# Optimization experiments

Hardware: AMD Instinct MI355X
Metric: run time of the kernel (lower is better)

Reference implementation:

```python
import jax, jax.numpy as jnp
import numpy as np

HEADS = 8
LN_EPS = 1e-5


def _elu_plus_one(t):
    # F.elu(x) + 1 == exp(x) for x<0, x+1 for x>=0
    return jax.nn.elu(t) + 1.0


def setup_inputs() -> dict:
    key = jax.random.key(0)
    k1, k2, k3 = jax.random.split(key, 3)
    dim = 256
    x = jax.random.normal(k1, (16, dim, 64, 64), dtype=jnp.float32)
    w_qkv = jax.random.normal(k2, (3 * dim, dim), dtype=jnp.float32) * 0.02
    w_out = jax.random.normal(k3, (dim, dim), dtype=jnp.float32) * 0.02
    ln_gamma = jnp.ones((dim,), dtype=jnp.float32)
    ln_beta = jnp.zeros((dim,), dtype=jnp.float32)
    return {"x": x, "w_qkv": w_qkv, "w_out": w_out, "ln_gamma": ln_gamma, "ln_beta": ln_beta}


def reference(x, w_qkv, w_out, ln_gamma, ln_beta):
    b, c, h, w = x.shape
    hd = c // HEADS
    n = h * w
    # 1x1 conv == per-pixel matmul over channels
    qkv = jnp.einsum('bchw,oc->bohw', x, w_qkv)  # [b, 3c, h, w]
    q, k, v = jnp.split(qkv, 3, axis=1)
    q = q.reshape(b, HEADS, hd, n)
    k = k.reshape(b, HEADS, hd, n)
    v = v.reshape(b, HEADS, hd, n)
    qk = _elu_plus_one(q)
    kk = _elu_plus_one(k)
    # channel-wise kv reduction over spatial positions (NOT an outer product)
    kv = jnp.sum(kk * v, axis=-1, keepdims=True)        # [b, heads, hd, 1]
    denom = jnp.maximum(jnp.sum(kk, axis=-1, keepdims=True), 1e-6)
    out = qk * (kv / denom)                              # [b, heads, hd, n]
    out = out.reshape(b, c, h, w)
    out = jnp.einsum('bchw,oc->bohw', out, w_out)        # 1x1 output conv
    # LayerNorm over channel dim (module permutes to NHWC first)
    t = jnp.transpose(out, (0, 2, 3, 1))                 # [b, h, w, c]
    mu = jnp.mean(t, axis=-1, keepdims=True)
    var = jnp.mean(jnp.square(t - mu), axis=-1, keepdims=True)
    t = (t - mu) * jax.lax.rsqrt(var + LN_EPS) * ln_gamma + ln_beta
    return jnp.transpose(t, (0, 3, 1, 2))
```

## Files before the change

### kernel.cpp

```cpp
#include <hip/hip_runtime.h>


#define NB 16
#define NC 256
#define NN 4096
#define LN_EPS 1e-5f
#define IOSCALE (1.0f/1024.0f)

typedef _Float16 f16;
typedef _Float16 f16x8 __attribute__((ext_vector_type(8)));
typedef _Float16 f16x4v __attribute__((ext_vector_type(4)));
typedef float f32x4 __attribute__((ext_vector_type(4)));

typedef __attribute__((address_space(1))) const unsigned int* as1cu32;
typedef __attribute__((address_space(3))) unsigned int* as3u32;

__device__ __forceinline__ void gload16(const void* g, void* l) {
  __builtin_amdgcn_global_load_lds((as1cu32)g, (as3u32)l, 16, 0, 0);
}

__device__ __forceinline__ float elu1(float x) {
  return x > 0.f ? x + 1.f : __expf(x);
}

__device__ __forceinline__ int swz(int row, int unit) {
  return row * 64 + (((unit) ^ (row & 7)) << 3);
}

__global__ __launch_bounds__(256) void k_init(const float* __restrict__ wqkv,
                                              const float* __restrict__ wout,
                                              f16* __restrict__ wh,
                                              f16* __restrict__ wouth,
                                              float* __restrict__ kvden) {
  int i = blockIdx.x * 256 + threadIdx.x;
  wh[i] = (f16)wqkv[i];
  if (i < 65536) wouth[i] = (f16)wout[i];
  if (i < 8192) kvden[i] = 0.f;
}

__global__ __launch_bounds__(256) void k_transpose(const float* __restrict__ x,
                                                   f16* __restrict__ xh) {
  __shared__ float t[64 * 65];
  const int b = blockIdx.z, c0 = blockIdx.y * 64, n0 = blockIdx.x * 64;
  const int tid = threadIdx.x;
#pragma unroll
  for (int i = 0; i < 4; ++i) {
    int lin = tid + i * 256;
    int r = lin >> 4;
    int cg = lin & 15;
    const float4 v = *reinterpret_cast<const float4*>(
        &x[((size_t)(b * NC + c0 + r)) * NN + n0 + cg * 4]);
    t[r * 65 + cg * 4 + 0] = v.x;
    t[r * 65 + cg * 4 + 1] = v.y;
    t[r * 65 + cg * 4 + 2] = v.z;
    t[r * 65 + cg * 4 + 3] = v.w;
  }
  __syncthreads();
#pragma unroll
  for (int i = 0; i < 4; ++i) {
    int lin = tid + i * 256;
    int nr = lin >> 4;
    int cg = lin & 15;
    f16x4v h;
    h[0] = (f16)t[(cg * 4 + 0) * 65 + nr];
    h[1] = (f16)t[(cg * 4 + 1) * 65 + nr];
    h[2] = (f16)t[(cg * 4 + 2) * 65 + nr];
    h[3] = (f16)t[(cg * 4 + 3) * 65 + nr];
    *reinterpret_cast<f16x4v*>(&xh[((size_t)(b * NN + n0 + nr)) * NC + c0 + cg * 4]) = h;
  }
}

__global__ __launch_bounds__(512) void k_kv(const f16* __restrict__ xh,
                                            const f16* __restrict__ wh,
                                            float* __restrict__ kv,
                                            float* __restrict__ den) {
  __shared__ __align__(16) f16 Xt[64 * 64];
  __shared__ __align__(16) f16 Bt[256 * 64];
  const int b = blockIdx.y;
  const int n0 = blockIdx.x * 64;
  const int tid = threadIdx.x;
  const int lane = tid & 63;
  const int wv = tid >> 6;
  const int ng = wv >> 2;
  const int cg = wv & 3;
  const int l15 = lane & 15, lg = lane >> 4;
  const int lr = lane >> 3;
  const int ssrc = ((lane & 7) ^ lr) * 8;

  f32x4 kacc[2][4] = {};
  f32x4 vacc[2][4] = {};

  for (int ks = 0; ks < 4; ++ks) {
    const int c0 = ks * 64;
    __syncthreads();
    gload16(xh + ((size_t)(b * NN + n0 + wv * 8 + lr)) * NC + c0 + ssrc, Xt + wv * 512);
#pragma unroll
    for (int it = 0; it < 4; ++it) {
      const int seg = wv * 4 + it;
      gload16(wh + (size_t)(256 + seg * 8 + lr) * NC + c0 + ssrc, Bt + seg * 512);
    }
    __syncthreads();
#pragma unroll
    for (int kk = 0; kk < 2; ++kk) {
      const int ku = kk * 4 + lg;
      f16x8 af[2], bf[4];
#pragma unroll
      for (int m = 0; m < 2; ++m)
        af[m] = *(const f16x8*)(Xt + swz(ng * 32 + m * 16 + l15, ku));
#pragma unroll
      for (int f = 0; f < 4; ++f)
        bf[f] = *(const f16x8*)(Bt + swz(cg * 64 + f * 16 + l15, ku));
#pragma unroll
      for (int m = 0; m < 2; ++m)
#pragma unroll
        for (int f = 0; f < 4; ++f)
          kacc[m][f] = __builtin_amdgcn_mfma_f32_16x16x32_f16(af[m], bf[f], kacc[m][f], 0, 0, 0);
    }
    __syncthreads();
#pragma unroll
    for (int it = 0; it < 4; ++it) {
      const int seg = wv * 4 + it;
      gload16(wh + (size_t)(512 + seg * 8 + lr) * NC + c0 + ssrc, Bt + seg * 512);
    }
    __syncthreads();
#pragma unroll
    for (int kk = 0; kk < 2; ++kk) {
      const int ku = kk * 4 + lg;
      f16x8 af[2], bf[4];
#pragma unroll
      for (int m = 0; m < 2; ++m)
        af[m] = *(const f16x8*)(Xt + swz(ng * 32 + m * 16 + l15, ku));
#pragma unroll
      for (int f = 0; f < 4; ++f)
        bf[f] = *(const f16x8*)(Bt + swz(cg * 64 + f * 16 + l15, ku));
#pragma unroll
      for (int m = 0; m < 2; ++m)
#pragma unroll
        for (int f = 0; f < 4; ++f)
          vacc[m][f] = __builtin_amdgcn_mfma_f32_16x16x32_f16(af[m], bf[f], vacc[m][f], 0, 0, 0);
    }
  }
  float pkv[4] = {0.f, 0.f, 0.f, 0.f}, pden[4] = {0.f, 0.f, 0.f, 0.f};
#pragma unroll
  for (int f = 0; f < 4; ++f)
#pragma unroll
    for (int m = 0; m < 2; ++m)
#pragma unroll
      for (int j = 0; j < 4; ++j) {
        const float kk = elu1(kacc[m][f][j]);
        pkv[f] += kk * vacc[m][f][j];
        pden[f] += kk;
      }
#pragma unroll
  for (int f = 0; f < 4; ++f) {
    pkv[f] += __shfl_xor(pkv[f], 16, 64);
    pkv[f] += __shfl_xor(pkv[f], 32, 64);
    pden[f] += __shfl_xor(pden[f], 16, 64);
    pden[f] += __shfl_xor(pden[f], 32, 64);
  }
  if (lane < 16) {
#pragma unroll
    for (int f = 0; f < 4; ++f) {
      const int c = cg * 64 + f * 16 + lane;
      atomicAdd(&kv[b * NC + c], pkv[f]);
      atomicAdd(&den[b * NC + c], pden[f]);
    }
  }
}

__global__ __launch_bounds__(256) void k_fused2(const f16* __restrict__ xh,
                                                const f16* __restrict__ wh,
                                                const f16* __restrict__ wouth,
                                                const float* __restrict__ kv,
                                                const float* __restrict__ den,
                                                const float* __restrict__ gamma,
                                                const float* __restrict__ beta,
                                                float* __restrict__ out) {
  __shared__ __align__(16) f16 Xt[64 * 64];
  __shared__ __align__(16) f16 Wt[256 * 64];
  __shared__ __align__(16) f16 Q[64 * 264];
  __shared__ float s1024[256];
  __shared__ float red1[4][64], red2[4][64];
  __shared__ float smu[64], srs[64];
  const int b = blockIdx.y;
  const int n0 = blockIdx.x * 64;
  const int tid = threadIdx.x;
  const int lane = tid & 63;
  const int wv = tid >> 6;
  const int l15 = lane & 15, lg = lane >> 4;
  const int lr = lane >> 3;
  const int ssrc = ((lane & 7) ^ lr) * 8;

  s1024[tid] = kv[b * NC + tid] / fmaxf(den[b * NC + tid], 1e-6f) * 1024.0f;

  f32x4 acc[4][4] = {};

  for (int ks = 0; ks < 4; ++ks) {
    const int c0 = ks * 64;
    __syncthreads();
#pragma unroll
    for (int it = 0; it < 2; ++it) {
      const int seg = wv * 2 + it;
      gload16(xh + ((size_t)(b * NN + n0 + seg * 8 + lr)) * NC + c0 + ssrc, Xt + seg * 512);
    }
#pragma unroll
    for (int it = 0; it < 8; ++it) {
      const int seg = wv * 8 + it;
      gload16(wh + (size_t)(seg * 8 + lr) * NC + c0 + ssrc, Wt + seg * 512);
    }
    __syncthreads();
#pragma unroll
    for (int kk = 0; kk < 2; ++kk) {
      const int ku = kk * 4 + lg;
      f16x8 af[4], bf[4];
#pragma unroll
      for (int m = 0; m < 4; ++m)
        af[m] = *(const f16x8*)(Wt + swz(wv * 64 + m * 16 + l15, ku));
#pragma unroll
      for (int f = 0; f < 4; ++f)
        bf[f] = *(const f16x8*)(Xt + swz(f * 16 + l15, ku));
#pragma unroll
      for (int m = 0; m < 4; ++m)
#pragma unroll
        for (int f = 0; f < 4; ++f)
          acc[m][f] = __builtin_amdgcn_mfma_f32_16x16x32_f16(af[m], bf[f], acc[m][f], 0, 0, 0);
    }
  }

#pragma unroll
  for (int m = 0; m < 4; ++m) {
    const int cq = wv * 64 + m * 16 + lg * 4;
#pragma unroll
    for (int f = 0; f < 4; ++f) {
      const int n = f * 16 + l15;
      f16x4v h;
#pragma unroll
      for (int j = 0; j < 4; ++j)
        h[j] = (f16)(elu1(acc[m][f][j]) * s1024[cq + j]);
      *reinterpret_cast<f16x4v*>(Q + n * 264 + cq) = h;
    }
  }

  f32x4 acc2[4][4] = {};
  for (int ks = 0; ks < 4; ++ks) {
    const int c0 = ks * 64;
    __syncthreads();
#pragma unroll
    for (int it = 0; it < 8; ++it) {
      const int seg = wv * 8 + it;
      gload16(wouth + (size_t)(seg * 8 + lr) * NC + c0 + ssrc, Wt + seg * 512);
    }
    __syncthreads();
#pragma unroll
    for (int kk = 0; kk < 2; ++kk) {
      const int ku = kk * 4 + lg;
      const int kb = c0 + kk * 32 + lg * 8;
      f16x8 af[4], bf[4];
#pragma unroll
      for (int m = 0; m < 4; ++m)
        af[m] = *(const f16x8*)(Wt + swz(wv * 64 + m * 16 + l15, ku));
#pragma unroll
      for (int f = 0; f < 4; ++f)
        bf[f] = *(const f16x8*)(Q + (f * 16 + l15) * 264 + kb);
#pragma unroll
      for (int m = 0; m < 4; ++m)
#pragma unroll
        for (int f = 0; f < 4; ++f)
          acc2[m][f] = __builtin_amdgcn_mfma_f32_16x16x32_f16(af[m], bf[f], acc2[m][f], 0, 0, 0);
    }
  }

  float s1[4] = {0, 0, 0, 0}, s2[4] = {0, 0, 0, 0};
#pragma unroll
  for (int f = 0; f < 4; ++f)
#pragma unroll
    for (int m = 0; m < 4; ++m)
#pragma unroll
      for (int j = 0; j < 4; ++j) {
        const float v = acc2[m][f][j];
        s1[f] += v;
        s2[f] += v * v;
      }
#pragma unroll
  for (int f = 0; f < 4; ++f) {
    s1[f] += __shfl_xor(s1[f], 16, 64);
    s1[f] += __shfl_xor(s1[f], 32, 64);
    s2[f] += __shfl_xor(s2[f], 16, 64);
    s2[f] += __shfl_xor(s2[f], 32, 64);
  }
  if (lane < 16) {
#pragma unroll
    for (int f = 0; f < 4; ++f) {
      red1[wv][f * 16 + lane] = s1[f];
      red2[wv][f * 16 + lane] = s2[f];
    }
  }
  __syncthreads();
  if (tid < 64) {
    const float a1 = red1[0][tid] + red1[1][tid] + red1[2][tid] + red1[3][tid];
    const float a2 = red2[0][tid] + red2[1][tid] + red2[2][tid] + red2[3][tid];
    const float mu = a1 * (IOSCALE / 256.f);
    const float e2 = a2 * (IOSCALE * IOSCALE / 256.f);
    smu[tid] = mu;
    srs[tid] = rsqrtf(e2 - mu * mu + LN_EPS);
  }
  __syncthreads();
#pragma unroll
  for (int m = 0; m < 4; ++m) {
    const int ob = wv * 64 + m * 16 + lg * 4;
#pragma unroll
    for (int j = 0; j < 4; ++j) {
      const int o = ob + j;
      const float g = gamma[o], be = beta[o];
#pragma unroll
      for (int f = 0; f < 4; ++f) {
        const int col = f * 16 + l15;
        const float v = acc2[m][f][j] * IOSCALE;
        out[((size_t)(b * NC + o)) * NN + n0 + col] = (v - smu[col]) * srs[col] * g + be;
      }
    }
  }
}

extern "C" void kernel_launch(void* const* d_in, const int* in_sizes, int n_in,
                              void* d_out, int out_size, void* d_ws, size_t ws_size,
                              hipStream_t stream) {
  const float* x = (const float*)d_in[0];
  const float* w_qkv = (const float*)d_in[1];
  const float* w_out = (const float*)d_in[2];
  const float* ln_g = (const float*)d_in[3];
  const float* ln_b = (const float*)d_in[4];
  float* out = (float*)d_out;

  char* wsb = (char*)d_ws;
  const size_t OFF_WH = 0;
  const size_t OFF_WOUTH = 393216;
  const size_t OFF_XH = OFF_WOUTH + 131072;
  const size_t OFF_KV = OFF_XH + 33554432;
  const size_t OFF_DEN = OFF_KV + 16384;

  f16* wh = (f16*)(wsb + OFF_WH);
  f16* wouth = (f16*)(wsb + OFF_WOUTH);
  f16* xh = (f16*)(wsb + OFF_XH);
  float* kv = (float*)(wsb + OFF_KV);
  float* den = (float*)(wsb + OFF_DEN);

  k_init<<<768, 256, 0, stream>>>(w_qkv, w_out, wh, wouth, kv);
  k_transpose<<<dim3(64, 4, 16), 256, 0, stream>>>(x, xh);
  k_kv<<<dim3(64, 16), 512, 0, stream>>>(xh, wh, kv, den);
  k_fused2<<<dim3(64, 16), 256, 0, stream>>>(xh, wh, wouth, kv, den, ln_g, ln_b, out);
}
```

Before: 84.87 us.

## Fuse transpose into kv kernel and widen fused output kernel to 512 threads

Removes the standalone transpose kernel. The kv kernel now reads fp32 x directly, converts it to f16 into a padded LDS tile holding all channels, writes the f16 transposed copy for later use, and feeds its MFMAs from that tile. This saves one launch and one round trip of xh through memory in the kv pass. The fused output kernel goes from 256 to 512 threads, splitting each block's work across channel groups and pixel halves, to raise parallelism and shrink per-thread accumulators. In exchange, the transposing LDS writes are scalar f16 stores that may hit bank conflicts.

```diff
diff --git a/kernel.cpp b/kernel.cpp
--- a/kernel.cpp
+++ b/kernel.cpp
@@ -38,43 +38,12 @@
   if (i < 8192) kvden[i] = 0.f;
 }
 
-__global__ __launch_bounds__(256) void k_transpose(const float* __restrict__ x,
-                                                   f16* __restrict__ xh) {
-  __shared__ float t[64 * 65];
-  const int b = blockIdx.z, c0 = blockIdx.y * 64, n0 = blockIdx.x * 64;
-  const int tid = threadIdx.x;
-#pragma unroll
-  for (int i = 0; i < 4; ++i) {
-    int lin = tid + i * 256;
-    int r = lin >> 4;
-    int cg = lin & 15;
-    const float4 v = *reinterpret_cast<const float4*>(
-        &x[((size_t)(b * NC + c0 + r)) * NN + n0 + cg * 4]);
-    t[r * 65 + cg * 4 + 0] = v.x;
-    t[r * 65 + cg * 4 + 1] = v.y;
-    t[r * 65 + cg * 4 + 2] = v.z;
-    t[r * 65 + cg * 4 + 3] = v.w;
-  }
-  __syncthreads();
-#pragma unroll
-  for (int i = 0; i < 4; ++i) {
-    int lin = tid + i * 256;
-    int nr = lin >> 4;
-    int cg = lin & 15;
-    f16x4v h;
-    h[0] = (f16)t[(cg * 4 + 0) * 65 + nr];
-    h[1] = (f16)t[(cg * 4 + 1) * 65 + nr];
-    h[2] = (f16)t[(cg * 4 + 2) * 65 + nr];
-    h[3] = (f16)t[(cg * 4 + 3) * 65 + nr];
-    *reinterpret_cast<f16x4v*>(&xh[((size_t)(b * NN + n0 + nr)) * NC + c0 + cg * 4]) = h;
-  }
-}
-
-__global__ __launch_bounds__(512) void k_kv(const f16* __restrict__ xh,
-                                            const f16* __restrict__ wh,
-                                            float* __restrict__ kv,
-                                            float* __restrict__ den) {
-  __shared__ __align__(16) f16 Xt[64 * 64];
+__global__ __launch_bounds__(512) void k_kvt(const float* __restrict__ x,
+                                             const f16* __restrict__ wh,
+                                             f16* __restrict__ xh,
+                                             float* __restrict__ kv,
+                                             float* __restrict__ den) {
+  __shared__ __align__(16) f16 Xt[64 * 264];
   __shared__ __align__(16) f16 Bt[256 * 64];
   const int b = blockIdx.y;
   const int n0 = blockIdx.x * 64;
@@ -87,13 +56,38 @@
   const int lr = lane >> 3;
   const int ssrc = ((lane & 7) ^ lr) * 8;
 
+  {
+    const int c = tid >> 1;
+    const int nh = (tid & 1) * 32;
+    const float* xp = x + ((size_t)(b * NC + c)) * NN + n0 + nh;
+#pragma unroll
+    for (int i = 0; i < 8; ++i) {
+      const float4 v4 = *reinterpret_cast<const float4*>(xp + i * 4);
+      const int nb = nh + i * 4;
+      Xt[(nb + 0) * 264 + c] = (f16)v4.x;
+      Xt[(nb + 1) * 264 + c] = (f16)v4.y;
+      Xt[(nb + 2) * 264 + c] = (f16)v4.z;
+      Xt[(nb + 3) * 264 + c] = (f16)v4.w;
+    }
+  }
+  __syncthreads();
+
+  {
+    const int r = tid >> 3;
+    const int s = (tid & 7) * 32;
+#pragma unroll
+    for (int q = 0; q < 4; ++q) {
+      const f16x8 h = *(const f16x8*)(Xt + r * 264 + s + q * 8);
+      *reinterpret_cast<f16x8*>(&xh[((size_t)(b * NN + n0 + r)) * NC + s + q * 8]) = h;
+    }
+  }
+
   f32x4 kacc[2][4] = {};
   f32x4 vacc[2][4] = {};
 
   for (int ks = 0; ks < 4; ++ks) {
     const int c0 = ks * 64;
     __syncthreads();
-    gload16(xh + ((size_t)(b * NN + n0 + wv * 8 + lr)) * NC + c0 + ssrc, Xt + wv * 512);
 #pragma unroll
     for (int it = 0; it < 4; ++it) {
       const int seg = wv * 4 + it;
@@ -103,10 +97,11 @@
 #pragma unroll
     for (int kk = 0; kk < 2; ++kk) {
       const int ku = kk * 4 + lg;
+      const int col = c0 + kk * 32 + lg * 8;
       f16x8 af[2], bf[4];
 #pragma unroll
       for (int m = 0; m < 2; ++m)
-        af[m] = *(const f16x8*)(Xt + swz(ng * 32 + m * 16 + l15, ku));
+        af[m] = *(const f16x8*)(Xt + (ng * 32 + m * 16 + l15) * 264 + col);
 #pragma unroll
       for (int f = 0; f < 4; ++f)
         bf[f] = *(const f16x8*)(Bt + swz(cg * 64 + f * 16 + l15, ku));
@@ -126,10 +121,11 @@
 #pragma unroll
     for (int kk = 0; kk < 2; ++kk) {
       const int ku = kk * 4 + lg;
+      const int col = c0 + kk * 32 + lg * 8;
       f16x8 af[2], bf[4];
 #pragma unroll
       for (int m = 0; m < 2; ++m)
-        af[m] = *(const f16x8*)(Xt + swz(ng * 32 + m * 16 + l15, ku));
+        af[m] = *(const f16x8*)(Xt + (ng * 32 + m * 16 + l15) * 264 + col);
 #pragma unroll
       for (int f = 0; f < 4; ++f)
         bf[f] = *(const f16x8*)(Bt + swz(cg * 64 + f * 16 + l15, ku));
@@ -168,7 +164,7 @@
   }
 }
 
-__global__ __launch_bounds__(256) void k_fused2(const f16* __restrict__ xh,
+__global__ __launch_bounds__(512) void k_fused2(const f16* __restrict__ xh,
                                                 const f16* __restrict__ wh,
                                                 const f16* __restrict__ wouth,
                                                 const float* __restrict__ kv,
@@ -176,8 +172,8 @@
                                                 const float* __restrict__ gamma,
                                                 const float* __restrict__ beta,
                                                 float* __restrict__ out) {
-  __shared__ __align__(16) f16 Xt[64 * 64];
   __shared__ __align__(16) f16 Wt[256 * 64];
+  __shared__ __align__(16) f16 Xc[64 * 64];
   __shared__ __align__(16) f16 Q[64 * 264];
   __shared__ float s1024[256];
   __shared__ float red1[4][64], red2[4][64];
@@ -187,52 +183,51 @@
   const int tid = threadIdx.x;
   const int lane = tid & 63;
   const int wv = tid >> 6;
+  const int cg = wv >> 1;
+  const int ng = wv & 1;
   const int l15 = lane & 15, lg = lane >> 4;
   const int lr = lane >> 3;
   const int ssrc = ((lane & 7) ^ lr) * 8;
 
-  s1024[tid] = kv[b * NC + tid] / fmaxf(den[b * NC + tid], 1e-6f) * 1024.0f;
-
-  f32x4 acc[4][4] = {};
+  if (tid < 256)
+    s1024[tid] = kv[b * NC + tid] / fmaxf(den[b * NC + tid], 1e-6f) * 1024.0f;
+
+  f32x4 acc[4][2] = {};
 
   for (int ks = 0; ks < 4; ++ks) {
     const int c0 = ks * 64;
     __syncthreads();
-#pragma unroll
-    for (int it = 0; it < 2; ++it) {
-      const int seg = wv * 2 + it;
-      gload16(xh + ((size_t)(b * NN + n0 + seg * 8 + lr)) * NC + c0 + ssrc, Xt + seg * 512);
-    }
-#pragma unroll
-    for (int it = 0; it < 8; ++it) {
-      const int seg = wv * 8 + it;
+    gload16(xh + ((size_t)(b * NN + n0 + wv * 8 + lr)) * NC + c0 + ssrc, Xc + wv * 512);
+#pragma unroll
+    for (int it = 0; it < 4; ++it) {
+      const int seg = wv * 4 + it;
       gload16(wh + (size_t)(seg * 8 + lr) * NC + c0 + ssrc, Wt + seg * 512);
     }
     __syncthreads();
 #pragma unroll
     for (int kk = 0; kk < 2; ++kk) {
       const int ku = kk * 4 + lg;
-      f16x8 af[4], bf[4];
+      f16x8 af[4], bf[2];
 #pragma unroll
       for (int m = 0; m < 4; ++m)
-        af[m] = *(const f16x8*)(Wt + swz(wv * 64 + m * 16 + l15, ku));
-#pragma unroll
-      for (int f = 0; f < 4; ++f)
-        bf[f] = *(const f16x8*)(Xt + swz(f * 16 + l15, ku));
+        af[m] = *(const f16x8*)(Wt + swz(cg * 64 + m * 16 + l15, ku));
+#pragma unroll
+      for (int f = 0; f < 2; ++f)
+        bf[f] = *(const f16x8*)(Xc + swz(ng * 32 + f * 16 + l15, ku));
 #pragma unroll
       for (int m = 0; m < 4; ++m)
 #pragma unroll
-        for (int f = 0; f < 4; ++f)
+        for (int f = 0; f < 2; ++f)
           acc[m][f] = __builtin_amdgcn_mfma_f32_16x16x32_f16(af[m], bf[f], acc[m][f], 0, 0, 0);
     }
   }
 
 #pragma unroll
   for (int m = 0; m < 4; ++m) {
-    const int cq = wv * 64 + m * 16 + lg * 4;
-#pragma unroll
-    for (int f = 0; f < 4; ++f) {
-      const int n = f * 16 + l15;
+    const int cq = cg * 64 + m * 16 + lg * 4;
+#pragma unroll
+    for (int f = 0; f < 2; ++f) {
+      const int n = ng * 32 + f * 16 + l15;
       f16x4v h;
 #pragma unroll
       for (int j = 0; j < 4; ++j)
@@ -241,13 +236,13 @@
     }
   }
 
-  f32x4 acc2[4][4] = {};
+  f32x4 acc2[4][2] = {};
   for (int ks = 0; ks < 4; ++ks) {
     const int c0 = ks * 64;
     __syncthreads();
 #pragma unroll
-    for (int it = 0; it < 8; ++it) {
-      const int seg = wv * 8 + it;
+    for (int it = 0; it < 4; ++it) {
+      const int seg = wv * 4 + it;
       gload16(wouth + (size_t)(seg * 8 + lr) * NC + c0 + ssrc, Wt + seg * 512);
     }
     __syncthreads();
@@ -255,24 +250,24 @@
     for (int kk = 0; kk < 2; ++kk) {
       const int ku = kk * 4 + lg;
       const int kb = c0 + kk * 32 + lg * 8;
-      f16x8 af[4], bf[4];
+      f16x8 af[4], bf[2];
 #pragma unroll
       for (int m = 0; m < 4; ++m)
-        af[m] = *(const f16x8*)(Wt + swz(wv * 64 + m * 16 + l15, ku));
-#pragma unroll
-      for (int f = 0; f < 4; ++f)
-        bf[f] = *(const f16x8*)(Q + (f * 16 + l15) * 264 + kb);
+        af[m] = *(const f16x8*)(Wt + swz(cg * 64 + m * 16 + l15, ku));
+#pragma unroll
+      for (int f = 0; f < 2; ++f)
+        bf[f] = *(const f16x8*)(Q + (ng * 32 + f * 16 + l15) * 264 + kb);
 #pragma unroll
       for (int m = 0; m < 4; ++m)
 #pragma unroll
-        for (int f = 0; f < 4; ++f)
+        for (int f = 0; f < 2; ++f)
           acc2[m][f] = __builtin_amdgcn_mfma_f32_16x16x32_f16(af[m], bf[f], acc2[m][f], 0, 0, 0);
     }
   }
 
-  float s1[4] = {0, 0, 0, 0}, s2[4] = {0, 0, 0, 0};
-#pragma unroll
-  for (int f = 0; f < 4; ++f)
+  float s1[2] = {0, 0}, s2[2] = {0, 0};
+#pragma unroll
+  for (int f = 0; f < 2; ++f)
 #pragma unroll
     for (int m = 0; m < 4; ++m)
 #pragma unroll
@@ -282,7 +277,7 @@
         s2[f] += v * v;
       }
 #pragma unroll
-  for (int f = 0; f < 4; ++f) {
+  for (int f = 0; f < 2; ++f) {
     s1[f] += __shfl_xor(s1[f], 16, 64);
     s1[f] += __shfl_xor(s1[f], 32, 64);
     s2[f] += __shfl_xor(s2[f], 16, 64);
@@ -290,9 +285,9 @@
   }
   if (lane < 16) {
 #pragma unroll
-    for (int f = 0; f < 4; ++f) {
-      red1[wv][f * 16 + lane] = s1[f];
-      red2[wv][f * 16 + lane] = s2[f];
+    for (int f = 0; f < 2; ++f) {
+      red1[cg][ng * 32 + f * 16 + lane] = s1[f];
+      red2[cg][ng * 32 + f * 16 + lane] = s2[f];
     }
   }
   __syncthreads();
@@ -307,14 +302,14 @@
   __syncthreads();
 #pragma unroll
   for (int m = 0; m < 4; ++m) {
-    const int ob = wv * 64 + m * 16 + lg * 4;
+    const int ob = cg * 64 + m * 16 + lg * 4;
 #pragma unroll
     for (int j = 0; j < 4; ++j) {
       const int o = ob + j;
       const float g = gamma[o], be = beta[o];
 #pragma unroll
-      for (int f = 0; f < 4; ++f) {
-        const int col = f * 16 + l15;
+      for (int f = 0; f < 2; ++f) {
+        const int col = ng * 32 + f * 16 + l15;
         const float v = acc2[m][f][j] * IOSCALE;
         out[((size_t)(b * NC + o)) * NN + n0 + col] = (v - smu[col]) * srs[col] * g + be;
       }
@@ -346,7 +341,6 @@
   float* den = (float*)(wsb + OFF_DEN);
 
   k_init<<<768, 256, 0, stream>>>(w_qkv, w_out, wh, wouth, kv);
-  k_transpose<<<dim3(64, 4, 16), 256, 0, stream>>>(x, xh);
-  k_kv<<<dim3(64, 16), 512, 0, stream>>>(xh, wh, kv, den);
-  k_fused2<<<dim3(64, 16), 256, 0, stream>>>(xh, wh, wouth, kv, den, ln_g, ln_b, out);
-}
+  k_kvt<<<dim3(64, 16), 512, 0, stream>>>(x, wh, xh, kv, den);
+  k_fused2<<<dim3(64, 16), 512, 0, stream>>>(xh, wh, wouth, kv, den, ln_g, ln_b, out);
+}
```

Measured after the change: 86.68 us. +2.1%, slower.

## Double-buffer K-chunks in kv and fused kernels, widen fused kernel to 512 threads

Applied to the files above, without the earlier changes.

Both GEMM kernels now stream the reduction dimension in 32-wide chunks through double-buffered LDS. The next chunk's global-to-LDS loads are issued before the current chunk's MFMAs, so one barrier per step replaces the earlier load/sync/compute/sync sequence. k_kv loads the K and V weight rows together so each X fragment feeds both products. k_fused2 goes to 512 threads split 4x2 over channels and pixels, prefetches the output weights during the last Q step, stores Q with an XOR swizzle instead of padding, and reuses the X buffer for the LayerNorm reductions. The aim is to hide memory latency and add occupancy, at the cost of smaller MFMA batches per barrier and more LDS use.

```diff
diff --git a/kernel.cpp b/kernel.cpp
--- a/kernel.cpp
+++ b/kernel.cpp
@@ -18,14 +18,10 @@
 __device__ __forceinline__ void gload16(const void* g, void* l) {
   __builtin_amdgcn_global_load_lds((as1cu32)g, (as3u32)l, 16, 0, 0);
 }
-
 __device__ __forceinline__ float elu1(float x) {
   return x > 0.f ? x + 1.f : __expf(x);
 }
-
-__device__ __forceinline__ int swz(int row, int unit) {
-  return row * 64 + (((unit) ^ (row & 7)) << 3);
-}
+#define MFMA16 __builtin_amdgcn_mfma_f32_16x16x32_f16
 
 __global__ __launch_bounds__(256) void k_init(const float* __restrict__ wqkv,
                                               const float* __restrict__ wout,
@@ -70,76 +66,61 @@
   }
 }
 
-__global__ __launch_bounds__(512) void k_kv(const f16* __restrict__ xh,
-                                            const f16* __restrict__ wh,
-                                            float* __restrict__ kv,
-                                            float* __restrict__ den) {
-  __shared__ __align__(16) f16 Xt[64 * 64];
-  __shared__ __align__(16) f16 Bt[256 * 64];
+__global__ __launch_bounds__(512, 4) void k_kv(const f16* __restrict__ xh,
+                                               const f16* __restrict__ wh,
+                                               float* __restrict__ kv,
+                                               float* __restrict__ den) {
+  __shared__ __align__(16) f16 Xc[2][64 * 32];
+  __shared__ __align__(16) f16 Bt[2][512 * 32];
   const int b = blockIdx.y;
   const int n0 = blockIdx.x * 64;
   const int tid = threadIdx.x;
   const int lane = tid & 63;
   const int wv = tid >> 6;
-  const int ng = wv >> 2;
-  const int cg = wv & 3;
+  const int ng = wv >> 2, cg = wv & 3;
   const int l15 = lane & 15, lg = lane >> 4;
-  const int lr = lane >> 3;
-  const int ssrc = ((lane & 7) ^ lr) * 8;
+  const int srow = lane >> 2;
+  const int scol = (((lane & 3) ^ (srow & 3)) * 8);
+  const int xu = ((lg ^ (l15 & 3)) << 3);
 
   f32x4 kacc[2][4] = {};
   f32x4 vacc[2][4] = {};
 
-  for (int ks = 0; ks < 4; ++ks) {
-    const int c0 = ks * 64;
-    __syncthreads();
-    gload16(xh + ((size_t)(b * NN + n0 + wv * 8 + lr)) * NC + c0 + ssrc, Xt + wv * 512);
-#pragma unroll
-    for (int it = 0; it < 4; ++it) {
-      const int seg = wv * 4 + it;
-      gload16(wh + (size_t)(256 + seg * 8 + lr) * NC + c0 + ssrc, Bt + seg * 512);
-    }
-    __syncthreads();
-#pragma unroll
-    for (int kk = 0; kk < 2; ++kk) {
-      const int ku = kk * 4 + lg;
-      f16x8 af[2], bf[4];
-#pragma unroll
-      for (int m = 0; m < 2; ++m)
-        af[m] = *(const f16x8*)(Xt + swz(ng * 32 + m * 16 + l15, ku));
-#pragma unroll
-      for (int f = 0; f < 4; ++f)
-        bf[f] = *(const f16x8*)(Bt + swz(cg * 64 + f * 16 + l15, ku));
-#pragma unroll
-      for (int m = 0; m < 2; ++m)
-#pragma unroll
-        for (int f = 0; f < 4; ++f)
-          kacc[m][f] = __builtin_amdgcn_mfma_f32_16x16x32_f16(af[m], bf[f], kacc[m][f], 0, 0, 0);
-    }
-    __syncthreads();
-#pragma unroll
-    for (int it = 0; it < 4; ++it) {
-      const int seg = wv * 4 + it;
-      gload16(wh + (size_t)(512 + seg * 8 + lr) * NC + c0 + ssrc, Bt + seg * 512);
-    }
-    __syncthreads();
-#pragma unroll
-    for (int kk = 0; kk < 2; ++kk) {
-      const int ku = kk * 4 + lg;
-      f16x8 af[2], bf[4];
-#pragma unroll
-      for (int m = 0; m < 2; ++m)
-        af[m] = *(const f16x8*)(Xt + swz(ng * 32 + m * 16 + l15, ku));
-#pragma unroll
-      for (int f = 0; f < 4; ++f)
-        bf[f] = *(const f16x8*)(Bt + swz(cg * 64 + f * 16 + l15, ku));
-#pragma unroll
-      for (int m = 0; m < 2; ++m)
-#pragma unroll
-        for (int f = 0; f < 4; ++f)
-          vacc[m][f] = __builtin_amdgcn_mfma_f32_16x16x32_f16(af[m], bf[f], vacc[m][f], 0, 0, 0);
-    }
-  }
+#pragma unroll
+  for (int i = 0; i < 4; ++i) {
+    const int inst = wv * 4 + i;
+    gload16(wh + (size_t)(256 + inst * 16 + srow) * NC + scol, &Bt[0][inst * 512]);
+  }
+  if (wv < 4)
+    gload16(xh + ((size_t)(b * NN + n0 + wv * 16 + srow)) * NC + scol, &Xc[0][wv * 512]);
+  __syncthreads();
+
+  for (int s = 0; s < 8; ++s) {
+    const int cb = s & 1, nb = (s + 1) & 1;
+    if (s < 7) {
+      const int c0 = (s + 1) * 32;
+#pragma unroll
+      for (int i = 0; i < 4; ++i) {
+        const int inst = wv * 4 + i;
+        gload16(wh + (size_t)(256 + inst * 16 + srow) * NC + c0 + scol, &Bt[nb][inst * 512]);
+      }
+      if (wv < 4)
+        gload16(xh + ((size_t)(b * NN + n0 + wv * 16 + srow)) * NC + c0 + scol, &Xc[nb][wv * 512]);
+    }
+    const f16x8 a0 = *(const f16x8*)(&Xc[cb][(ng * 32 + l15) * 32 + xu]);
+    const f16x8 a1 = *(const f16x8*)(&Xc[cb][(ng * 32 + 16 + l15) * 32 + xu]);
+#pragma unroll
+    for (int f = 0; f < 4; ++f) {
+      const f16x8 bk = *(const f16x8*)(&Bt[cb][(cg * 64 + f * 16 + l15) * 32 + xu]);
+      kacc[0][f] = MFMA16(a0, bk, kacc[0][f], 0, 0, 0);
+      kacc[1][f] = MFMA16(a1, bk, kacc[1][f], 0, 0, 0);
+      const f16x8 bv = *(const f16x8*)(&Bt[cb][(256 + cg * 64 + f * 16 + l15) * 32 + xu]);
+      vacc[0][f] = MFMA16(a0, bv, vacc[0][f], 0, 0, 0);
+      vacc[1][f] = MFMA16(a1, bv, vacc[1][f], 0, 0, 0);
+    }
+    if (s < 7) __syncthreads();
+  }
+
   float pkv[4] = {0.f, 0.f, 0.f, 0.f}, pden[4] = {0.f, 0.f, 0.f, 0.f};
 #pragma unroll
   for (int f = 0; f < 4; ++f)
@@ -168,111 +149,132 @@
   }
 }
 
-__global__ __launch_bounds__(256) void k_fused2(const f16* __restrict__ xh,
-                                                const f16* __restrict__ wh,
-                                                const f16* __restrict__ wouth,
-                                                const float* __restrict__ kv,
-                                                const float* __restrict__ den,
-                                                const float* __restrict__ gamma,
-                                                const float* __restrict__ beta,
-                                                float* __restrict__ out) {
-  __shared__ __align__(16) f16 Xt[64 * 64];
-  __shared__ __align__(16) f16 Wt[256 * 64];
-  __shared__ __align__(16) f16 Q[64 * 264];
-  __shared__ float s1024[256];
-  __shared__ float red1[4][64], red2[4][64];
-  __shared__ float smu[64], srs[64];
+__global__ __launch_bounds__(512, 4) void k_fused2(const f16* __restrict__ xh,
+                                                   const f16* __restrict__ wh,
+                                                   const f16* __restrict__ wouth,
+                                                   const float* __restrict__ kv,
+                                                   const float* __restrict__ den,
+                                                   const float* __restrict__ gamma,
+                                                   const float* __restrict__ beta,
+                                                   float* __restrict__ out) {
+  __shared__ __align__(16) f16 Xc[2][64 * 32];
+  __shared__ __align__(16) f16 Wt[2][256 * 32];
+  __shared__ __align__(16) f16 Q[64 * 256];
   const int b = blockIdx.y;
   const int n0 = blockIdx.x * 64;
   const int tid = threadIdx.x;
   const int lane = tid & 63;
   const int wv = tid >> 6;
+  const int cg = wv >> 1, ng = wv & 1;
   const int l15 = lane & 15, lg = lane >> 4;
-  const int lr = lane >> 3;
-  const int ssrc = ((lane & 7) ^ lr) * 8;
-
-  s1024[tid] = kv[b * NC + tid] / fmaxf(den[b * NC + tid], 1e-6f) * 1024.0f;
-
-  f32x4 acc[4][4] = {};
-
-  for (int ks = 0; ks < 4; ++ks) {
-    const int c0 = ks * 64;
-    __syncthreads();
-#pragma unroll
-    for (int it = 0; it < 2; ++it) {
-      const int seg = wv * 2 + it;
-      gload16(xh + ((size_t)(b * NN + n0 + seg * 8 + lr)) * NC + c0 + ssrc, Xt + seg * 512);
-    }
-#pragma unroll
-    for (int it = 0; it < 8; ++it) {
-      const int seg = wv * 8 + it;
-      gload16(wh + (size_t)(seg * 8 + lr) * NC + c0 + ssrc, Wt + seg * 512);
-    }
-    __syncthreads();
-#pragma unroll
-    for (int kk = 0; kk < 2; ++kk) {
-      const int ku = kk * 4 + lg;
-      f16x8 af[4], bf[4];
-#pragma unroll
-      for (int m = 0; m < 4; ++m)
-        af[m] = *(const f16x8*)(Wt + swz(wv * 64 + m * 16 + l15, ku));
-#pragma unroll
-      for (int f = 0; f < 4; ++f)
-        bf[f] = *(const f16x8*)(Xt + swz(f * 16 + l15, ku));
-#pragma unroll
-      for (int m = 0; m < 4; ++m)
-#pragma unroll
-        for (int f = 0; f < 4; ++f)
-          acc[m][f] = __builtin_amdgcn_mfma_f32_16x16x32_f16(af[m], bf[f], acc[m][f], 0, 0, 0);
-    }
+  const int srow = lane >> 2;
+  const int scol = (((lane & 3) ^ (srow & 3)) * 8);
+  const int xu = ((lg ^ (l15 & 3)) << 3);
+
+  float sreg[4][4];
+#pragma unroll
+  for (int m = 0; m < 4; ++m)
+#pragma unroll
+    for (int j = 0; j < 4; ++j) {
+      const int c = cg * 64 + m * 16 + lg * 4 + j;
+      sreg[m][j] = kv[b * NC + c] / fmaxf(den[b * NC + c], 1e-6f) * 1024.0f;
+    }
+
+#pragma unroll
+  for (int i = 0; i < 2; ++i) {
+    const int inst = wv * 2 + i;
+    gload16(wh + (size_t)(inst * 16 + srow) * NC + scol, &Wt[0][inst * 512]);
+  }
+  if (wv < 4)
+    gload16(xh + ((size_t)(b * NN + n0 + wv * 16 + srow)) * NC + scol, &Xc[0][wv * 512]);
+  __syncthreads();
+
+  f32x4 acc[4][2] = {};
+  for (int s = 0; s < 8; ++s) {
+    const int cb = s & 1, nb = (s + 1) & 1;
+    if (s < 7) {
+      const int c0 = (s + 1) * 32;
+#pragma unroll
+      for (int i = 0; i < 2; ++i) {
+        const int inst = wv * 2 + i;
+        gload16(wh + (size_t)(inst * 16 + srow) * NC + c0 + scol, &Wt[nb][inst * 512]);
+      }
+      if (wv < 4)
+        gload16(xh + ((size_t)(b * NN + n0 + wv * 16 + srow)) * NC + c0 + scol, &Xc[nb][wv * 512]);
+    } else {
+#pragma unroll
+      for (int i = 0; i < 2; ++i) {
+        const int inst = wv * 2 + i;
+        gload16(wouth + (size_t)(inst * 16 + srow) * NC + scol, &Wt[nb][inst * 512]);
+      }
+    }
+    f16x8 a[4], bx[2];
+#pragma unroll
+    for (int m = 0; m < 4; ++m)
+      a[m] = *(const f16x8*)(&Wt[cb][(cg * 64 + m * 16 + l15) * 32 + xu]);
+#pragma unroll
+    for (int f = 0; f < 2; ++f)
+      bx[f] = *(const f16x8*)(&Xc[cb][(ng * 32 + f * 16 + l15) * 32 + xu]);
+#pragma unroll
+    for (int m = 0; m < 4; ++m)
+#pragma unroll
+      for (int f = 0; f < 2; ++f)
+        acc[m][f] = MFMA16(a[m], bx[f], acc[m][f], 0, 0, 0);
+    if (s < 7) __syncthreads();
   }
 
 #pragma unroll
   for (int m = 0; m < 4; ++m) {
-    const int cq = wv * 64 + m * 16 + lg * 4;
-#pragma unroll
-    for (int f = 0; f < 4; ++f) {
-      const int n = f * 16 + l15;
+#pragma unroll
+    for (int f = 0; f < 2; ++f) {
+      const int n = ng * 32 + f * 16 + l15;
+      const int ch = cg * 64 + m * 16 + lg * 4;
+      const int u = ch >> 3;
       f16x4v h;
 #pragma unroll
       for (int j = 0; j < 4; ++j)
-        h[j] = (f16)(elu1(acc[m][f][j]) * s1024[cq + j]);
-      *reinterpret_cast<f16x4v*>(Q + n * 264 + cq) = h;
-    }
-  }
-
-  f32x4 acc2[4][4] = {};
-  for (int ks = 0; ks < 4; ++ks) {
-    const int c0 = ks * 64;
-    __syncthreads();
-#pragma unroll
-    for (int it = 0; it < 8; ++it) {
-      const int seg = wv * 8 + it;
-      gload16(wouth + (size_t)(seg * 8 + lr) * NC + c0 + ssrc, Wt + seg * 512);
-    }
-    __syncthreads();
-#pragma unroll
-    for (int kk = 0; kk < 2; ++kk) {
-      const int ku = kk * 4 + lg;
-      const int kb = c0 + kk * 32 + lg * 8;
-      f16x8 af[4], bf[4];
-#pragma unroll
-      for (int m = 0; m < 4; ++m)
-        af[m] = *(const f16x8*)(Wt + swz(wv * 64 + m * 16 + l15, ku));
-#pragma unroll
-      for (int f = 0; f < 4; ++f)
-        bf[f] = *(const f16x8*)(Q + (f * 16 + l15) * 264 + kb);
-#pragma unroll
-      for (int m = 0; m < 4; ++m)
-#pragma unroll
-        for (int f = 0; f < 4; ++f)
-          acc2[m][f] = __builtin_amdgcn_mfma_f32_16x16x32_f16(af[m], bf[f], acc2[m][f], 0, 0, 0);
-    }
-  }
-
-  float s1[4] = {0, 0, 0, 0}, s2[4] = {0, 0, 0, 0};
-#pragma unroll
-  for (int f = 0; f < 4; ++f)
+        h[j] = (f16)(elu1(acc[m][f][j]) * sreg[m][j]);
+      *reinterpret_cast<f16x4v*>(&Q[n * 256 + ((u ^ (n & 7)) << 3) + (ch & 7)]) = h;
+    }
+  }
+  __syncthreads();
+
+  f32x4 acc2[4][2] = {};
+  for (int s = 0; s < 8; ++s) {
+    const int cb = s & 1, nb = (s + 1) & 1;
+    if (s < 7) {
+      const int c0 = (s + 1) * 32;
+#pragma unroll
+      for (int i = 0; i < 2; ++i) {
+        const int inst = wv * 2 + i;
+        gload16(wouth + (size_t)(inst * 16 + srow) * NC + c0 + scol, &Wt[nb][inst * 512]);
+      }
+    }
+    f16x8 a[4], bq[2];
+#pragma unroll
+    for (int m = 0; m < 4; ++m)
+      a[m] = *(const f16x8*)(&Wt[cb][(cg * 64 + m * 16 + l15) * 32 + xu]);
+#pragma unroll
+    for (int f = 0; f < 2; ++f) {
+      const int n = ng * 32 + f * 16 + l15;
+      const int U = s * 4 + lg;
+      bq[f] = *(const f16x8*)(&Q[n * 256 + ((U ^ (n & 7)) << 3)]);
+    }
+#pragma unroll
+    for (int m = 0; m < 4; ++m)
+#pragma unroll
+      for (int f = 0; f < 2; ++f)
+        acc2[m][f] = MFMA16(a[m], bq[f], acc2[m][f], 0, 0, 0);
+    if (s < 7) __syncthreads();
+  }
+
+  float* red1 = (float*)(&Xc[0][0]);
+  float* red2 = red1 + 256;
+  float* smu = red2 + 256;
+  float* srs = smu + 64;
+  float s1[2] = {0, 0}, s2[2] = {0, 0};
+#pragma unroll
+  for (int f = 0; f < 2; ++f)
 #pragma unroll
     for (int m = 0; m < 4; ++m)
 #pragma unroll
@@ -282,23 +284,24 @@
         s2[f] += v * v;
       }
 #pragma unroll
-  for (int f = 0; f < 4; ++f) {
+  for (int f = 0; f < 2; ++f) {
     s1[f] += __shfl_xor(s1[f], 16, 64);
     s1[f] += __shfl_xor(s1[f], 32, 64);
     s2[f] += __shfl_xor(s2[f], 16, 64);
     s2[f] += __shfl_xor(s2[f], 32, 64);
   }
+  __syncthreads();
   if (lane < 16) {
 #pragma unroll
-    for (int f = 0; f < 4; ++f) {
-      red1[wv][f * 16 + lane] = s1[f];
-      red2[wv][f * 16 + lane] = s2[f];
+    for (int f = 0; f < 2; ++f) {
+      red1[cg * 64 + ng * 32 + f * 16 + lane] = s1[f];
+      red2[cg * 64 + ng * 32 + f * 16 + lane] = s2[f];
     }
   }
   __syncthreads();
   if (tid < 64) {
-    const float a1 = red1[0][tid] + red1[1][tid] + red1[2][tid] + red1[3][tid];
-    const float a2 = red2[0][tid] + red2[1][tid] + red2[2][tid] + red2[3][tid];
+    const float a1 = red1[tid] + red1[64 + tid] + red1[128 + tid] + red1[192 + tid];
+    const float a2 = red2[tid] + red2[64 + tid] + red2[128 + tid] + red2[192 + tid];
     const float mu = a1 * (IOSCALE / 256.f);
     const float e2 = a2 * (IOSCALE * IOSCALE / 256.f);
     smu[tid] = mu;
@@ -307,14 +310,14 @@
   __syncthreads();
 #pragma unroll
   for (int m = 0; m < 4; ++m) {
-    const int ob = wv * 64 + m * 16 + lg * 4;
+    const int ob = cg * 64 + m * 16 + lg * 4;
 #pragma unroll
     for (int j = 0; j < 4; ++j) {
       const int o = ob + j;
       const float g = gamma[o], be = beta[o];
 #pragma unroll
-      for (int f = 0; f < 4; ++f) {
-        const int col = f * 16 + l15;
+      for (int f = 0; f < 2; ++f) {
+        const int col = ng * 32 + f * 16 + l15;
         const float v = acc2[m][f][j] * IOSCALE;
         out[((size_t)(b * NC + o)) * NN + n0 + col] = (v - smu[col]) * srs[col] * g + be;
       }
@@ -348,5 +351,5 @@
   k_init<<<768, 256, 0, stream>>>(w_qkv, w_out, wh, wouth, kv);
   k_transpose<<<dim3(64, 4, 16), 256, 0, stream>>>(x, xh);
   k_kv<<<dim3(64, 16), 512, 0, stream>>>(xh, wh, kv, den);
-  k_fused2<<<dim3(64, 16), 256, 0, stream>>>(xh, wh, wouth, kv, den, ln_g, ln_b, out);
-}
+  k_fused2<<<dim3(64, 16), 512, 0, stream>>>(xh, wh, wouth, kv, den, ln_g, ln_b, out);
+}
```

Measured after the change: 94.43 us. 1.11x slower.
